# Performance work log

Measured on AMD Instinct MI355X. Metric: run time of the kernel, lower is better.

The kernel has to match this reference:

```python
import jax, jax.numpy as jnp
import numpy as np

N_NODES = 100000
N_EDGES = 1600000
D_IN = 13      # per-localization feature dim
D_POS = 3
HIDDEN = 64
D_OUT = 64


def setup_inputs() -> dict:
    key = jax.random.key(0)
    ks = jax.random.split(key, 6)
    x_locs = jax.random.normal(ks[0], (N_NODES, D_IN), dtype=jnp.float32)
    pos_locs = jax.random.uniform(ks[1], (N_NODES, D_POS), dtype=jnp.float32)
    edge_index = jax.random.randint(ks[2], (2, N_EDGES), 0, N_NODES, dtype=jnp.int64)
    fan1 = D_IN + D_POS
    W1 = jax.random.normal(ks[3], (fan1, HIDDEN), dtype=jnp.float32) / np.sqrt(fan1)
    b1 = jnp.zeros((HIDDEN,), dtype=jnp.float32)
    W2 = jax.random.normal(ks[4], (HIDDEN, D_OUT), dtype=jnp.float32) / np.sqrt(HIDDEN)
    b2 = jnp.zeros((D_OUT,), dtype=jnp.float32)
    return {"x_locs": x_locs, "pos_locs": pos_locs, "W1": W1, "b1": b1,
            "W2": W2, "b2": b2, "edge_index": edge_index}


def reference(x_locs, pos_locs, W1, b1, W2, b2, edge_index):
    # PointNetConv (source_to_target): j = edge_index[0] (source), i = edge_index[1] (target)
    src = edge_index[0]
    dst = edge_index[1]
    # message input: [x_j, pos_j - pos_i]  -> [E, D_IN + D_POS]
    msg_in = jnp.concatenate([x_locs[src], pos_locs[src] - pos_locs[dst]], axis=-1)
    # local_nn: Linear -> ReLU -> Linear
    h = jax.nn.relu(msg_in @ W1 + b1)            # [E, HIDDEN]
    h = h @ W2 + b2                               # [E, D_OUT]
    # max aggregation per target node; empty segments get -inf
    agg = jax.ops.segment_max(h, dst, num_segments=N_NODES)  # [N, D_OUT]
    # final .relu() in LocEncoder; also maps empty (-inf) segments to 0 (PyG convention)
    return jax.nn.relu(agg)
```

## Files before the change

kernel.cpp:

```cpp
#include <hip/hip_runtime.h>
#include <hip/hip_bf16.h>


#define N_NODES 100000
#define N_EDGES 1600000
#define NB2  782
#define NBLK 391
#define BATCH 4096
#define SCAP 2400

typedef short short8  __attribute__((ext_vector_type(8)));
typedef float float4v __attribute__((ext_vector_type(4)));

__device__ inline short f2bf(float f) {
    union { float f; unsigned u; } v; v.f = f;
    unsigned u = v.u;
    u += 0x7fffu + ((u >> 16) & 1u);
    return (short)(u >> 16);
}
__device__ inline short2 f2bf2(float a, float b) {
    __hip_bfloat162 h = __float22bfloat162_rn(make_float2(a, b));
    return *(short2*)&h;
}
__device__ inline float bf2f(short s) {
    union { unsigned u; float f; } v;
    v.u = ((unsigned)(unsigned short)s) << 16;
    return v.f;
}
__device__ inline int wave_incl_scan(int v, int lane) {
#pragma unroll
    for (int d = 1; d < 64; d <<= 1) {
        const int t = __shfl_up(v, d);
        if (lane >= d) v += t;
    }
    return v;
}

__global__ __launch_bounds__(256) void prep_kernel(
    const float* __restrict__ x, const float* __restrict__ pos,
    const float* __restrict__ W1, const float* __restrict__ b1,
    const int* __restrict__ ei,
    int* __restrict__ offsT,
    int* __restrict__ blockSorted,
    unsigned short* __restrict__ u16, unsigned short* __restrict__ w16)
{
    __shared__ int hist[NB2], eoff[NB2], offc[NB2];
    __shared__ int csumP[13];

    const int tid  = threadIdx.x;
    const int lane = tid & 63;
    const int wv   = tid >> 6;

    if (blockIdx.x >= NBLK) {
        float w1c[16];
#pragma unroll
        for (int k = 0; k < 16; ++k) w1c[k] = W1[k * 64 + lane];
        const float b1c = b1[lane];

        const int waveId = (blockIdx.x - NBLK) * 4 + wv;
        const int nwave  = 512 * 4;

        for (int node = waveId; node < N_NODES; node += nwave) {
            float m = 0.f;
            if (lane < 13) m = x[node * 13 + lane];
            else if (lane < 16) m = pos[node * 3 + (lane - 13)];

            float acc = b1c, accw = 0.f;
#pragma unroll
            for (int k = 0; k < 13; ++k)
                acc = fmaf(__shfl(m, k), w1c[k], acc);
#pragma unroll
            for (int k = 13; k < 16; ++k) {
                const float p = __shfl(m, k);
                acc  = fmaf(p, w1c[k], acc);
                accw = fmaf(p, w1c[k], accw);
            }
            u16[node * 64 + lane] = (unsigned short)f2bf(acc);
            w16[node * 64 + lane] = (unsigned short)f2bf(accw);
        }
        return;
    }

    const int blk = blockIdx.x;
    const int e0  = blk * BATCH;
    const int nn  = (N_EDGES - e0) < BATCH ? (N_EDGES - e0) : BATCH;

    for (int i = tid; i < NB2; i += 256) hist[i] = 0;
    __syncthreads();

#pragma unroll
    for (int rep = 0; rep < 4; ++rep) {
        const int base = rep * 1024 + tid * 4;
        if (base < nn) {
            const int4 d4 = *(const int4*)(ei + N_EDGES + e0 + base);
            atomicAdd(&hist[d4.x >> 7], 1);
            atomicAdd(&hist[d4.y >> 7], 1);
            atomicAdd(&hist[d4.z >> 7], 1);
            atomicAdd(&hist[d4.w >> 7], 1);
        }
    }
    __syncthreads();

    for (int c = wv; c < 13; c += 4) {
        const int idx = c * 64 + lane;
        const int val = (idx < NB2) ? hist[idx] : 0;
        const int inc = wave_incl_scan(val, lane);
        if (idx < NB2) eoff[idx] = inc;
        if (lane == 63) csumP[c] = inc;
    }
    __syncthreads();
    if (tid == 0) {
        int a = 0;
#pragma unroll
        for (int c = 0; c < 13; ++c) { const int t = csumP[c]; csumP[c] = a; a += t; }
    }
    __syncthreads();
    for (int c = wv; c < 13; c += 4) {
        const int idx = c * 64 + lane;
        if (idx < NB2) eoff[idx] += csumP[c] - hist[idx];
    }
    __syncthreads();

    for (int b = tid; b < NB2; b += 256) {
        offsT[b * NBLK + blk] = eoff[b];
        offc[b] = eoff[b];
    }
    if (tid == 0) offsT[NB2 * NBLK + blk] = nn;
    __syncthreads();

    int* dstp = blockSorted + blk * BATCH;
#pragma unroll
    for (int rep = 0; rep < 4; ++rep) {
        const int base = rep * 1024 + tid * 4;
        if (base < nn) {
            const int4 s4 = *(const int4*)(ei + e0 + base);
            const int4 d4 = *(const int4*)(ei + N_EDGES + e0 + base);
            int p;
            p = atomicAdd(&offc[d4.x >> 7], 1); dstp[p] = (s4.x << 7) | (d4.x & 127);
            p = atomicAdd(&offc[d4.y >> 7], 1); dstp[p] = (s4.y << 7) | (d4.y & 127);
            p = atomicAdd(&offc[d4.z >> 7], 1); dstp[p] = (s4.z << 7) | (d4.z & 127);
            p = atomicAdd(&offc[d4.w >> 7], 1); dstp[p] = (s4.w << 7) | (d4.w & 127);
        }
    }
}

__global__ __launch_bounds__(256, 3) void aggregate_kernel(
    const unsigned short* __restrict__ u16,
    const unsigned short* __restrict__ w16,
    const float* __restrict__ W2,
    const float* __restrict__ b2,
    const int*   __restrict__ offsT,
    const int*   __restrict__ blockSorted,
    float*       __restrict__ out)
{
    __shared__ int accS[128 * 65];
    __shared__ int staged[SCAP + 16];
    __shared__ int E[NBLK], G[NBLK];
    __shared__ int csum[8];
    __shared__ int totT;

    const int tid  = threadIdx.x;
    const int lane = tid & 63;
    const int wv   = tid >> 6;
    const int q = lane >> 4, n = lane & 15;
    const int b = blockIdx.x;
    const int node0  = b * 128;
    const int nvalid = (N_NODES - node0) < 128 ? (N_NODES - node0) : 128;

    short8 w2f[2][4];
#pragma unroll
    for (int s = 0; s < 2; ++s)
#pragma unroll
        for (int t = 0; t < 4; ++t)
#pragma unroll
            for (int j = 0; j < 8; ++j)
                w2f[s][t][j] = f2bf(W2[(s * 32 + q * 8 + j) * 64 + (n + 16 * t)]);
    float b2c[4];
#pragma unroll
    for (int t = 0; t < 4; ++t) b2c[t] = b2[n + 16 * t];

    for (int i = tid; i < 128 * 65; i += 256) accS[i] = 0;

    for (int r = tid; r < NBLK; r += 256) {
        const int lo = offsT[b * NBLK + r];
        const int hi = offsT[(b + 1) * NBLK + r];
        staged[r] = hi - lo;
        G[r] = r * BATCH + lo;
    }
    __syncthreads();
    for (int c = wv; c < 7; c += 4) {
        const int idx = c * 64 + lane;
        const int val = (idx < NBLK) ? staged[idx] : 0;
        const int inc = wave_incl_scan(val, lane);
        if (idx < NBLK) E[idx] = inc;
        if (lane == 63) csum[c] = inc;
    }
    __syncthreads();
    if (tid == 0) {
        int a = 0;
#pragma unroll
        for (int c = 0; c < 7; ++c) { const int t = csum[c]; csum[c] = a; a += t; }
        totT = a;
    }
    __syncthreads();
    for (int c = wv; c < 7; c += 4) {
        const int idx = c * 64 + lane;
        if (idx < NBLK) E[idx] += csum[c] - staged[idx];
    }
    __syncthreads();

    int T = totT; T = T < SCAP ? T : SCAP;

    for (int i = tid; i < T; i += 256) {
        int lo = 0, hi = NBLK - 1;
#pragma unroll
        for (int s = 0; s < 9; ++s) {
            const int mid = (lo + hi + 1) >> 1;
            if (E[mid] <= i) lo = mid; else hi = mid - 1;
        }
        staged[i] = blockSorted[G[lo] + (i - E[lo])];
    }
    for (int i = T + tid; i < T + 16; i += 256) staged[i] = 0;
    __syncthreads();

    const int tiles = (T + 15) >> 4;

    auto load_tile = [&](int tile, int& wd, short8& ulo, short8& uhi,
                         short8& wl, short8& wh) {
        const int e  = tile * 16 + n;
        wd = staged[e];
        const bool ev = (e < T);
        const int src = ev ? (wd >> 7) : 0;
        const int dln = ev ? (wd & 127) : 0;
        ulo = *(const short8*)(u16 + src * 64 + q * 8);
        uhi = *(const short8*)(u16 + src * 64 + 32 + q * 8);
        wl  = *(const short8*)(w16 + (node0 + dln) * 64 + q * 8);
        wh  = *(const short8*)(w16 + (node0 + dln) * 64 + 32 + q * 8);
    };

    int tile = wv;
    int wd; short8 ulo, uhi, wl, wh;
    if (tile < tiles) load_tile(tile, wd, ulo, uhi, wl, wh);

    for (; tile < tiles; ) {
        const int tile2 = tile + 4;
        int wd2; short8 ulo2, uhi2, wl2, wh2;
        if (tile2 < tiles) load_tile(tile2, wd2, ulo2, uhi2, wl2, wh2);

        union { short8 v; short2 h[4]; } alo, ahi;
#pragma unroll
        for (int j = 0; j < 4; ++j) {
            alo.h[j] = f2bf2(fmaxf(bf2f(ulo[2*j])   - bf2f(wl[2*j]),   0.f),
                             fmaxf(bf2f(ulo[2*j+1]) - bf2f(wl[2*j+1]), 0.f));
            ahi.h[j] = f2bf2(fmaxf(bf2f(uhi[2*j])   - bf2f(wh[2*j]),   0.f),
                             fmaxf(bf2f(uhi[2*j+1]) - bf2f(wh[2*j+1]), 0.f));
        }

        float4v c2[4];
#pragma unroll
        for (int t = 0; t < 4; ++t) {
            c2[t] = __builtin_amdgcn_mfma_f32_16x16x32_bf16(
                alo.v, w2f[0][t], (float4v){0.f, 0.f, 0.f, 0.f}, 0, 0, 0);
            c2[t] = __builtin_amdgcn_mfma_f32_16x16x32_bf16(
                ahi.v, w2f[1][t], c2[t], 0, 0, 0);
        }

        const int rowbase = tile * 16 + q * 4;
        const int4 dw = *(const int4*)&staged[rowbase];
        const int dr[4] = {dw.x & 127, dw.y & 127, dw.z & 127, dw.w & 127};
#pragma unroll
        for (int r = 0; r < 4; ++r) {
            const bool rv = (rowbase + r) < T;
#pragma unroll
            for (int t = 0; t < 4; ++t) {
                const float v = c2[t][r] + b2c[t];
                if (rv && v > 0.f)
                    atomicMax(&accS[dr[r] * 65 + n + 16 * t], __float_as_int(v));
            }
        }

        tile = tile2;
        wd = wd2; ulo = ulo2; uhi = uhi2; wl = wl2; wh = wh2;
    }
    __syncthreads();

    for (int i = tid; i < nvalid * 64; i += 256) {
        const int row = i >> 6, col = i & 63;
        out[(node0 + row) * 64 + col] = __int_as_float(accS[row * 65 + col]);
    }
}

extern "C" void kernel_launch(void* const* d_in, const int* in_sizes, int n_in,
                              void* d_out, int out_size, void* d_ws, size_t ws_size,
                              hipStream_t stream) {
    const float* x   = (const float*)d_in[0];
    const float* pos = (const float*)d_in[1];
    const float* W1  = (const float*)d_in[2];
    const float* b1  = (const float*)d_in[3];
    const float* W2  = (const float*)d_in[4];
    const float* b2  = (const float*)d_in[5];
    const int*   ei  = (const int*)d_in[6];

    char* ws = (char*)d_ws;
    int* blockSorted = (int*)(ws + 0);
    int* offsT       = (int*)(ws + 6406144);
    unsigned short* u16 = (unsigned short*)(ws + 7631360);
    unsigned short* w16 = (unsigned short*)(ws + 20431360);

    prep_kernel<<<NBLK + 512, 256, 0, stream>>>(
        x, pos, W1, b1, ei, offsT, blockSorted, u16, w16);
    aggregate_kernel<<<NB2, 256, 0, stream>>>(
        u16, w16, W2, b2, offsT, blockSorted, (float*)d_out);
}
```

Before: 218.8 us.

## Sort edges per destination in LDS and reduce max in registers per node

Replaces the shared-memory atomicMax accumulator with a local counting sort of each block's edges by destination node. Each wave then handles 32 nodes, computes the MLP for up to 16 edges per node per MFMA tile, and reduces the max across lanes with shuffles. This removes the large accS array and its atomics, which allows 4 blocks per CU. The cost is that nodes with few edges waste MFMA rows, since 16 edges average per node gives poor tile utilization when degrees vary. Node processing is also serialized within a wave.

```diff
diff --git a/kernel.cpp b/kernel.cpp
--- a/kernel.cpp
+++ b/kernel.cpp
@@ -144,7 +144,7 @@
     }
 }
 
-__global__ __launch_bounds__(256, 3) void aggregate_kernel(
+__global__ __launch_bounds__(256, 4) void aggregate_kernel(
     const unsigned short* __restrict__ u16,
     const unsigned short* __restrict__ w16,
     const float* __restrict__ W2,
@@ -153,9 +153,10 @@
     const int*   __restrict__ blockSorted,
     float*       __restrict__ out)
 {
-    __shared__ int accS[128 * 65];
-    __shared__ int staged[SCAP + 16];
+    __shared__ int staged[SCAP];
+    __shared__ int sortedL[SCAP];
     __shared__ int E[NBLK], G[NBLK];
+    __shared__ int hist[128], hoff[128], nstart[128];
     __shared__ int csum[8];
     __shared__ int totT;
 
@@ -164,8 +165,7 @@
     const int wv   = tid >> 6;
     const int q = lane >> 4, n = lane & 15;
     const int b = blockIdx.x;
-    const int node0  = b * 128;
-    const int nvalid = (N_NODES - node0) < 128 ? (N_NODES - node0) : 128;
+    const int node0 = b * 128;
 
     short8 w2f[2][4];
 #pragma unroll
@@ -179,7 +179,7 @@
 #pragma unroll
     for (int t = 0; t < 4; ++t) b2c[t] = b2[n + 16 * t];
 
-    for (int i = tid; i < 128 * 65; i += 256) accS[i] = 0;
+    if (tid < 128) hist[tid] = 0;
 
     for (int r = tid; r < NBLK; r += 256) {
         const int lo = offsT[b * NBLK + r];
@@ -218,75 +218,110 @@
             const int mid = (lo + hi + 1) >> 1;
             if (E[mid] <= i) lo = mid; else hi = mid - 1;
         }
-        staged[i] = blockSorted[G[lo] + (i - E[lo])];
-    }
-    for (int i = T + tid; i < T + 16; i += 256) staged[i] = 0;
-    __syncthreads();
-
-    const int tiles = (T + 15) >> 4;
-
-    auto load_tile = [&](int tile, int& wd, short8& ulo, short8& uhi,
-                         short8& wl, short8& wh) {
-        const int e  = tile * 16 + n;
-        wd = staged[e];
-        const bool ev = (e < T);
-        const int src = ev ? (wd >> 7) : 0;
-        const int dln = ev ? (wd & 127) : 0;
-        ulo = *(const short8*)(u16 + src * 64 + q * 8);
-        uhi = *(const short8*)(u16 + src * 64 + 32 + q * 8);
-        wl  = *(const short8*)(w16 + (node0 + dln) * 64 + q * 8);
-        wh  = *(const short8*)(w16 + (node0 + dln) * 64 + 32 + q * 8);
+        const int w = blockSorted[G[lo] + (i - E[lo])];
+        staged[i] = w;
+        atomicAdd(&hist[w & 127], 1);
+    }
+    __syncthreads();
+
+    if (wv < 2) {
+        const int v = hist[tid];
+        const int inc = wave_incl_scan(v, lane);
+        nstart[tid] = inc - v;
+        if (lane == 63) csum[wv] = inc;
+    }
+    __syncthreads();
+    if (tid >= 64 && tid < 128) nstart[tid] += csum[0];
+    __syncthreads();
+    if (tid < 128) hoff[tid] = nstart[tid];
+    __syncthreads();
+    for (int i = tid; i < T; i += 256) {
+        const int w = staged[i];
+        const int p = atomicAdd(&hoff[w & 127], 1);
+        sortedL[p] = w >> 7;
+    }
+    __syncthreads();
+
+    auto compute = [&](int node, int2 sd, int src,
+                       short8 ulo, short8 uhi, short8 wl, short8 wh) {
+        float vmax[4] = {0.f, 0.f, 0.f, 0.f};
+        int base = 0;
+        while (true) {
+            const int rows = (sd.y - base) < 16 ? (sd.y - base) : 16;
+            if (rows > 0) {
+                union { short8 v; short2 h[4]; } alo, ahi;
+#pragma unroll
+                for (int j = 0; j < 4; ++j) {
+                    alo.h[j] = f2bf2(
+                        fmaxf(bf2f(ulo[2*j])   - bf2f(wl[2*j]),   0.f),
+                        fmaxf(bf2f(ulo[2*j+1]) - bf2f(wl[2*j+1]), 0.f));
+                    ahi.h[j] = f2bf2(
+                        fmaxf(bf2f(uhi[2*j])   - bf2f(wh[2*j]),   0.f),
+                        fmaxf(bf2f(uhi[2*j+1]) - bf2f(wh[2*j+1]), 0.f));
+                }
+                float4v c2[4];
+#pragma unroll
+                for (int t = 0; t < 4; ++t) {
+                    c2[t] = __builtin_amdgcn_mfma_f32_16x16x32_bf16(
+                        alo.v, w2f[0][t], (float4v){0.f, 0.f, 0.f, 0.f}, 0, 0, 0);
+                    c2[t] = __builtin_amdgcn_mfma_f32_16x16x32_bf16(
+                        ahi.v, w2f[1][t], c2[t], 0, 0, 0);
+                }
+#pragma unroll
+                for (int r = 0; r < 4; ++r) {
+                    const int row = q * 4 + r;
+#pragma unroll
+                    for (int t = 0; t < 4; ++t) {
+                        const float v = c2[t][r] + b2c[t];
+                        if (row < rows) vmax[t] = fmaxf(vmax[t], v);
+                    }
+                }
+            }
+            base += 16;
+            if (base >= sd.y) break;
+            const int r2 = (sd.y - base) < 16 ? (sd.y - base) : 16;
+            src = (n < r2) ? sortedL[sd.x + base + n] : 0;
+            ulo = *(const short8*)(u16 + src * 64 + q * 8);
+            uhi = *(const short8*)(u16 + src * 64 + 32 + q * 8);
+        }
+#pragma unroll
+        for (int t = 0; t < 4; ++t) {
+            vmax[t] = fmaxf(vmax[t], __shfl_xor(vmax[t], 16));
+            vmax[t] = fmaxf(vmax[t], __shfl_xor(vmax[t], 32));
+        }
+        float v = vmax[0];
+        v = (q == 1) ? vmax[1] : v;
+        v = (q == 2) ? vmax[2] : v;
+        v = (q == 3) ? vmax[3] : v;
+        if (node < N_NODES) out[node * 64 + lane] = v;
     };
 
-    int tile = wv;
-    int wd; short8 ulo, uhi, wl, wh;
-    if (tile < tiles) load_tile(tile, wd, ulo, uhi, wl, wh);
-
-    for (; tile < tiles; ) {
-        const int tile2 = tile + 4;
-        int wd2; short8 ulo2, uhi2, wl2, wh2;
-        if (tile2 < tiles) load_tile(tile2, wd2, ulo2, uhi2, wl2, wh2);
-
-        union { short8 v; short2 h[4]; } alo, ahi;
-#pragma unroll
-        for (int j = 0; j < 4; ++j) {
-            alo.h[j] = f2bf2(fmaxf(bf2f(ulo[2*j])   - bf2f(wl[2*j]),   0.f),
-                             fmaxf(bf2f(ulo[2*j+1]) - bf2f(wl[2*j+1]), 0.f));
-            ahi.h[j] = f2bf2(fmaxf(bf2f(uhi[2*j])   - bf2f(wh[2*j]),   0.f),
-                             fmaxf(bf2f(uhi[2*j+1]) - bf2f(wh[2*j+1]), 0.f));
-        }
-
-        float4v c2[4];
-#pragma unroll
-        for (int t = 0; t < 4; ++t) {
-            c2[t] = __builtin_amdgcn_mfma_f32_16x16x32_bf16(
-                alo.v, w2f[0][t], (float4v){0.f, 0.f, 0.f, 0.f}, 0, 0, 0);
-            c2[t] = __builtin_amdgcn_mfma_f32_16x16x32_bf16(
-                ahi.v, w2f[1][t], c2[t], 0, 0, 0);
-        }
-
-        const int rowbase = tile * 16 + q * 4;
-        const int4 dw = *(const int4*)&staged[rowbase];
-        const int dr[4] = {dw.x & 127, dw.y & 127, dw.z & 127, dw.w & 127};
-#pragma unroll
-        for (int r = 0; r < 4; ++r) {
-            const bool rv = (rowbase + r) < T;
-#pragma unroll
-            for (int t = 0; t < 4; ++t) {
-                const float v = c2[t][r] + b2c[t];
-                if (rv && v > 0.f)
-                    atomicMax(&accS[dr[r] * 65 + n + 16 * t], __float_as_int(v));
-            }
-        }
-
-        tile = tile2;
-        wd = wd2; ulo = ulo2; uhi = uhi2; wl = wl2; wh = wh2;
-    }
-    __syncthreads();
-
-    for (int i = tid; i < nvalid * 64; i += 256) {
-        const int row = i >> 6, col = i & 63;
-        out[(node0 + row) * 64 + col] = __int_as_float(accS[row * 65 + col]);
+    const int nlbase = wv * 32;
+#pragma unroll 1
+    for (int g = 0; g < 32; g += 2) {
+        const int nlA = nlbase + g, nlB = nlA + 1;
+        const int nA = node0 + nlA, nB = node0 + nlB;
+        const int2 sdA = {nstart[nlA], hist[nlA]};
+        const int2 sdB = {nstart[nlB], hist[nlB]};
+        const int nAc = nA < (N_NODES - 1) ? nA : (N_NODES - 1);
+        const int nBc = nB < (N_NODES - 1) ? nB : (N_NODES - 1);
+
+        const int rA = sdA.y < 16 ? sdA.y : 16;
+        const int rB = sdB.y < 16 ? sdB.y : 16;
+        const int srcA = (n < rA) ? sortedL[sdA.x + n] : 0;
+        const int srcB = (n < rB) ? sortedL[sdB.x + n] : 0;
+
+        const short8 ulA = *(const short8*)(u16 + srcA * 64 + q * 8);
+        const short8 uhA = *(const short8*)(u16 + srcA * 64 + 32 + q * 8);
+        const short8 wlA = *(const short8*)(w16 + nAc * 64 + q * 8);
+        const short8 whA = *(const short8*)(w16 + nAc * 64 + 32 + q * 8);
+        const short8 ulB = *(const short8*)(u16 + srcB * 64 + q * 8);
+        const short8 uhB = *(const short8*)(u16 + srcB * 64 + 32 + q * 8);
+        const short8 wlB = *(const short8*)(w16 + nBc * 64 + q * 8);
+        const short8 whB = *(const short8*)(w16 + nBc * 64 + 32 + q * 8);
+
+        compute(nA, sdA, srcA, ulA, uhA, wlA, whA);
+        compute(nB, sdB, srcB, ulB, uhB, wlB, whB);
     }
 }
 
```

Result: faster. 213.1 us (-2.6%).
